# Kernel tuning notes

Hardware: AMD Instinct MI355X
Metric: run time of the kernel (lower is better)

The kernel has to match this reference:

```python
import jax, jax.numpy as jnp
import numpy as np
from math import ceil


def _cubic(x, scale):
    # MATLAB-style antialiased cubic (Keys a=-0.5), scale <= 1
    x = np.asarray(x, dtype=np.float64) * scale
    ax = np.abs(x)
    ax2 = ax * ax
    ax3 = ax2 * ax
    w = (1.5 * ax3 - 2.5 * ax2 + 1.0) * (ax <= 1) + \
        (-0.5 * ax3 + 2.5 * ax2 - 4.0 * ax + 2.0) * ((ax > 1) & (ax <= 2))
    return w * scale


def _make_kernel(in_len, out_len):
    # Mirrors kernel() in the source: returns (taps[L], (pad_l, pad_r), stride).
    assert in_len >= out_len and in_len % out_len == 0
    scale = float(out_len) / float(in_len)
    klen = 4.0 / scale
    x = np.array([1, out_len], dtype=np.float64)
    u = x / scale + 0.5 * (1.0 - 1.0 / scale)
    left = np.floor(u - klen / 2.0)
    p = int(ceil(klen)) + 2
    ind = left[:, None] + np.arange(p) - 1
    indices = ind.astype(np.int64)
    weights = _cubic(u[:, None] - indices - 1, scale)
    weights = weights / weights.sum(axis=1, keepdims=True)
    keep = np.nonzero(np.any(weights, axis=0))[0]
    weights = weights[:, keep]
    indices = indices[:, keep]
    assert np.all(weights[0] == weights[-1])  # shift-invariant for integer stride
    pad_l = int(np.where(indices[0] == 0)[0][0])
    pad_r = indices.shape[1] - 1 - int(np.where(indices[-1] == in_len - 1)[0][0])
    return weights[0].astype(np.float32), (pad_l, pad_r), in_len // out_len


def setup_inputs() -> dict:
    key = jax.random.key(0)
    k1, k2 = jax.random.split(key)
    B, C, h, H = 32, 3, 128, 512
    inp = jax.random.uniform(k1, (B, C, h, h), dtype=jnp.float32)
    out = jax.random.uniform(k2, (B, C, H, H), dtype=jnp.float32)
    return {"input": inp, "output": out}


def reference(input, output):
    B, C, h, w = input.shape
    H, W = output.shape[2], output.shape[3]
    kh, ph, sh = _make_kernel(H, h)
    kw, pw, sw = _make_kernel(W, w)
    L = kh.shape[0]

    x = output.reshape(B * C, 1, H, W)  # depthwise via flattened channels
    # vertical pass: symmetric pad rows, conv with [L,1] kernel, stride (sh,1)
    x = jnp.pad(x, ((0, 0), (0, 0), (ph[0], ph[1]), (0, 0)), mode="symmetric")
    x = jax.lax.conv_general_dilated(
        x, jnp.asarray(kh).reshape(1, 1, L, 1), window_strides=(sh, 1),
        padding="VALID")
    # horizontal pass: symmetric pad cols, conv with [1,L] kernel, stride (1,sw)
    x = jnp.pad(x, ((0, 0), (0, 0), (0, 0), (pw[0], pw[1])), mode="symmetric")
    x = jax.lax.conv_general_dilated(
        x, jnp.asarray(kw).reshape(1, 1, 1, L), window_strides=(1, sw),
        padding="VALID")

    output_down = x.reshape(B, C, h, w)
    return jnp.mean(jnp.abs(output_down - input))
```

## Files before the change

kernel.cpp:

```cpp
#include <hip/hip_runtime.h>
#include <math.h>

#define BCN   96
#define IN_H  512
#define IN_W  512
#define OUT_H 128
#define OUT_W 128
#define TAPS  16
#define PAD   6
#define STRIDE 4
#define TR    8
#define IR    ((TR - 1) * STRIDE + TAPS)
#define NBLK  (BCN * (OUT_H / TR))
#define TOTAL_ELEMS (BCN * OUT_H * OUT_W)

struct K16 { float w[TAPS]; };

__device__ __forceinline__ int sym_idx(int i, int n) {
    i = (i < 0) ? (-1 - i) : i;
    i = (i >= n) ? (2 * n - 1 - i) : i;
    return i;
}

__global__ __launch_bounds__(256)
void bploss_kernel(const float* __restrict__ input,
                   const float* __restrict__ outimg,
                   float* __restrict__ loss, K16 kw)
{
    __shared__ float hbuf[IR * OUT_W];
    __shared__ float wsum[4];

    const int tid  = threadIdx.x;
    const int bc   = blockIdx.x >> 4;
    const int tile = blockIdx.x & 15;
    const int r0   = tile * TR;
    const int iy0  = r0 * STRIDE - PAD;

    const float* img = outimg + (size_t)bc * IN_H * IN_W;

    #pragma unroll 2
    for (int f = tid; f < IR * OUT_W; f += 256) {
        const int rr = f >> 7;
        const int xo = f & 127;
        const int y  = sym_idx(iy0 + rr, IN_H);
        const float* row = img + (size_t)y * IN_W;
        const int xb = xo * STRIDE - PAD;
        float acc = 0.0f;
        if (xb >= 0 && xb + TAPS <= IN_W) {
            const float2* p = reinterpret_cast<const float2*>(row + xb);
            #pragma unroll
            for (int t = 0; t < TAPS / 2; ++t) {
                float2 v = p[t];
                acc += kw.w[2 * t] * v.x + kw.w[2 * t + 1] * v.y;
            }
        } else {
            #pragma unroll
            for (int t = 0; t < TAPS; ++t) {
                const int x = sym_idx(xb + t, IN_W);
                acc += kw.w[t] * row[x];
            }
        }
        hbuf[f] = acc;
    }
    __syncthreads();

    float lsum = 0.0f;
    #pragma unroll
    for (int it = 0; it < (TR * OUT_W) / 256; ++it) {
        const int g  = tid + it * 256;
        const int yl = g >> 7;
        const int x  = g & 127;
        const float* hb = &hbuf[yl * STRIDE * OUT_W + x];
        float acc = 0.0f;
        #pragma unroll
        for (int t = 0; t < TAPS; ++t) acc += kw.w[t] * hb[t * OUT_W];
        const int yo = r0 + yl;
        const float ref = input[((size_t)bc * OUT_H + yo) * OUT_W + x];
        lsum += fabsf(acc - ref);
    }

    #pragma unroll
    for (int off = 32; off > 0; off >>= 1)
        lsum += __shfl_down(lsum, off, 64);

    const int wid = tid >> 6, lane = tid & 63;
    if (lane == 0) wsum[wid] = lsum;
    __syncthreads();
    if (tid == 0) {
        const float s = wsum[0] + wsum[1] + wsum[2] + wsum[3];
        atomicAdd(loss, s * (1.0f / (float)TOTAL_ELEMS));
    }
}

static void make_weights(K16* kw) {
    const double scale = 0.25;
    double w[TAPS]; double s = 0.0;
    for (int t = 0; t < TAPS; ++t) {
        const double ax = fabs((7.5 - (double)t) * scale);
        double v;
        if (ax <= 1.0)      v = 1.5 * ax * ax * ax - 2.5 * ax * ax + 1.0;
        else if (ax <= 2.0) v = -0.5 * ax * ax * ax + 2.5 * ax * ax - 4.0 * ax + 2.0;
        else                v = 0.0;
        w[t] = v * scale; s += w[t];
    }
    for (int t = 0; t < TAPS; ++t) kw->w[t] = (float)(w[t] / s);
}

extern "C" void kernel_launch(void* const* d_in, const int* in_sizes, int n_in,
                              void* d_out, int out_size, void* d_ws, size_t ws_size,
                              hipStream_t stream) {
    const float* input;
    const float* outimg;
    if (in_sizes[0] == TOTAL_ELEMS) {
        input  = (const float*)d_in[0];
        outimg = (const float*)d_in[1];
    } else {
        input  = (const float*)d_in[1];
        outimg = (const float*)d_in[0];
    }
    float* loss = (float*)d_out;

    K16 kw;
    make_weights(&kw);

    hipMemsetAsync(d_out, 0, sizeof(float), stream);
    bploss_kernel<<<NBLK, 256, 0, stream>>>(input, outimg, loss, kw);
}
```

Before: 186.0 us.

## Stage input rows through double-buffered swizzled LDS with streaming vertical accumulation

Replaces direct global gathers for the horizontal pass with coalesced float4 loads of 4-row chunks into a double-buffered, XOR-swizzled shared buffer. Global loads for the next chunk are prefetched while the current chunk is processed. Each thread computes two horizontal outputs from a 24-float window. Vertical accumulation is streamed per chunk into registers instead of keeping the full intermediate tile in LDS. This targets redundant, uncoalesced global reads, at the cost of two barriers per chunk and special-case edge handling.

```diff
diff --git a/kernel.cpp b/kernel.cpp
--- a/kernel.cpp
+++ b/kernel.cpp
@@ -11,6 +11,7 @@
 #define STRIDE 4
 #define TR    8
 #define IR    ((TR - 1) * STRIDE + TAPS)
+#define NCH   (IR / 4)
 #define NBLK  (BCN * (OUT_H / TR))
 #define TOTAL_ELEMS (BCN * OUT_H * OUT_W)
 
@@ -18,16 +19,19 @@
 
 __device__ __forceinline__ int sym_idx(int i, int n) {
     i = (i < 0) ? (-1 - i) : i;
-    i = (i >= n) ? (2 * n - 1 - i) : i;
-    return i;
+    return (i >= n) ? (2 * n - 1 - i) : i;
 }
+
+__device__ __forceinline__ int swz(int b) { return b ^ (((b >> 7) & 1) << 4); }
 
 __global__ __launch_bounds__(256)
 void bploss_kernel(const float* __restrict__ input,
                    const float* __restrict__ outimg,
-                   float* __restrict__ loss, K16 kw)
+                   float* __restrict__ loss, K16 kwa)
 {
-    __shared__ float hbuf[IR * OUT_W];
+    __shared__ float dbuf[2][4 * IN_W];
+    __shared__ float hrow[4][OUT_W];
+    __shared__ float kwl[TAPS];
     __shared__ float wsum[4];
 
     const int tid  = threadIdx.x;
@@ -38,45 +42,103 @@
 
     const float* img = outimg + (size_t)bc * IN_H * IN_W;
 
-    #pragma unroll 2
-    for (int f = tid; f < IR * OUT_W; f += 256) {
-        const int rr = f >> 7;
-        const int xo = f & 127;
-        const int y  = sym_idx(iy0 + rr, IN_H);
-        const float* row = img + (size_t)y * IN_W;
-        const int xb = xo * STRIDE - PAD;
-        float acc = 0.0f;
-        if (xb >= 0 && xb + TAPS <= IN_W) {
-            const float2* p = reinterpret_cast<const float2*>(row + xb);
-            #pragma unroll
-            for (int t = 0; t < TAPS / 2; ++t) {
-                float2 v = p[t];
-                acc += kw.w[2 * t] * v.x + kw.w[2 * t + 1] * v.y;
-            }
-        } else {
+    auto gsrc = [&](int ch, int s) -> const float4* {
+        const int y = sym_idx(iy0 + ch * 4 + (s >> 7), IN_H);
+        return reinterpret_cast<const float4*>(img + (size_t)y * IN_W + (s & 127) * 4);
+    };
+    auto lslot = [&](float* buf, int s) -> float4* {
+        return reinterpret_cast<float4*>(reinterpret_cast<char*>(buf) + swz(s << 4));
+    };
+
+    {
+        float4 a = *gsrc(0, tid);
+        float4 b = *gsrc(0, tid + 256);
+        *lslot(dbuf[0], tid)       = a;
+        *lslot(dbuf[0], tid + 256) = b;
+    }
+    if (tid < TAPS) kwl[tid] = kwa.w[tid];
+    __syncthreads();
+
+    const int pr = tid >> 6;
+    const int c  = tid & 63;
+    const int vb = tid >> 7;
+    const int vx = tid & 127;
+
+    int f0 = 8 * c - 8;
+    f0 = (f0 < 0) ? 0 : f0;
+    f0 = (f0 > 488) ? 488 : f0;
+    const int Lbase = pr * (IN_W * 4) + f0 * 4;
+
+    float vacc[4] = {0.f, 0.f, 0.f, 0.f};
+
+    for (int ch = 0; ch < NCH; ++ch) {
+        const int chn = (ch + 1 < NCH) ? (ch + 1) : (NCH - 1);
+        const float4 n0 = *gsrc(chn, tid);
+        const float4 n1 = *gsrc(chn, tid + 256);
+
+        const char* raw = reinterpret_cast<const char*>(dbuf[ch & 1]);
+        const float4 w0 = *reinterpret_cast<const float4*>(raw + swz(Lbase));
+        const float4 w1 = *reinterpret_cast<const float4*>(raw + swz(Lbase + 16));
+        const float4 w2 = *reinterpret_cast<const float4*>(raw + swz(Lbase + 32));
+        const float4 w3 = *reinterpret_cast<const float4*>(raw + swz(Lbase + 48));
+        const float4 w4 = *reinterpret_cast<const float4*>(raw + swz(Lbase + 64));
+        const float4 w5 = *reinterpret_cast<const float4*>(raw + swz(Lbase + 80));
+        const float win[24] = { w0.x,w0.y,w0.z,w0.w, w1.x,w1.y,w1.z,w1.w,
+                                w2.x,w2.y,w2.z,w2.w, w3.x,w3.y,w3.z,w3.w,
+                                w4.x,w4.y,w4.z,w4.w, w5.x,w5.y,w5.z,w5.w };
+        float acc0 = 0.f, acc1 = 0.f;
+        #pragma unroll
+        for (int t = 0; t < TAPS; ++t) {
+            acc0 += kwa.w[t] * win[t + 2];
+            acc1 += kwa.w[t] * win[t + 6];
+        }
+        if (c == 0) {
+            float a0 = 0.f, a1 = 0.f;
             #pragma unroll
             for (int t = 0; t < TAPS; ++t) {
-                const int x = sym_idx(xb + t, IN_W);
-                acc += kw.w[t] * row[x];
+                const int i0 = (t < 6) ? (5 - t) : (t - 6);
+                const int i1 = (t < 2) ? (1 - t) : (t - 2);
+                a0 += kwa.w[t] * win[i0];
+                a1 += kwa.w[t] * win[i1];
+            }
+            acc0 = a0; acc1 = a1;
+        } else if (c == 63) {
+            float a0 = 0.f, a1 = 0.f;
+            #pragma unroll
+            for (int t = 0; t < TAPS; ++t) {
+                const int i0 = (t <= 13) ? (10 + t) : ((t == 14) ? 23 : 22);
+                const int i1 = (t <= 9) ? (14 + t) : (33 - t);
+                a0 += kwa.w[t] * win[i0];
+                a1 += kwa.w[t] * win[i1];
+            }
+            acc0 = a0; acc1 = a1;
+        }
+        *reinterpret_cast<float2*>(&hrow[pr][2 * c]) = make_float2(acc0, acc1);
+
+        __syncthreads();
+
+        const float h0 = hrow[0][vx], h1 = hrow[1][vx],
+                    h2 = hrow[2][vx], h3 = hrow[3][vx];
+        #pragma unroll
+        for (int k = 0; k < 4; ++k) {
+            const int t0 = 4 * (ch - (4 * vb + k));
+            if (t0 >= 0 && t0 < TAPS) {
+                vacc[k] += kwl[t0] * h0 + kwl[t0 + 1] * h1
+                         + kwl[t0 + 2] * h2 + kwl[t0 + 3] * h3;
             }
         }
-        hbuf[f] = acc;
+
+        *lslot(dbuf[(ch + 1) & 1], tid)       = n0;
+        *lslot(dbuf[(ch + 1) & 1], tid + 256) = n1;
+        __syncthreads();
     }
-    __syncthreads();
 
-    float lsum = 0.0f;
+    float lsum = 0.f;
     #pragma unroll
-    for (int it = 0; it < (TR * OUT_W) / 256; ++it) {
-        const int g  = tid + it * 256;
-        const int yl = g >> 7;
-        const int x  = g & 127;
-        const float* hb = &hbuf[yl * STRIDE * OUT_W + x];
-        float acc = 0.0f;
-        #pragma unroll
-        for (int t = 0; t < TAPS; ++t) acc += kw.w[t] * hb[t * OUT_W];
-        const int yo = r0 + yl;
-        const float ref = input[((size_t)bc * OUT_H + yo) * OUT_W + x];
-        lsum += fabsf(acc - ref);
+    for (int k = 0; k < 4; ++k) {
+        const int yo = r0 + 4 * vb + k;
+        const float ref = input[((size_t)bc * OUT_H + yo) * OUT_W + vx];
+        lsum += fabsf(vacc[k] - ref);
     }
 
     #pragma unroll
```

New measurement: 170.5 us. 8.3% less time.
